# Performance work log

Hardware: AMD Instinct MI355X
Metric: run time of the kernel (lower is better)

## Reference

```python
import jax, jax.numpy as jnp
import numpy as np

H = 8  # pinyin_feature_size = embedding_dim = GRU hidden size
VOCAB = 27


def setup_inputs() -> dict:
    key = jax.random.key(0)
    ks = jax.random.split(key, 10)
    B, T = 131072, 24
    inputs = jax.random.randint(ks[0], (B, T), 0, VOCAB, dtype=jnp.int32)
    emb = jax.random.normal(ks[1], (VOCAB, H), dtype=jnp.float32)
    emb = emb.at[0].set(0.0)  # padding_idx=0
    s = 0.25  # ~ 1/sqrt(hidden) init scale like torch GRU
    w_ih1 = jax.random.normal(ks[2], (3 * H, H), dtype=jnp.float32) * s
    w_hh1 = jax.random.normal(ks[3], (3 * H, H), dtype=jnp.float32) * s
    b_ih1 = jax.random.normal(ks[4], (3 * H,), dtype=jnp.float32) * s
    b_hh1 = jax.random.normal(ks[5], (3 * H,), dtype=jnp.float32) * s
    w_ih2 = jax.random.normal(ks[6], (3 * H, H), dtype=jnp.float32) * s
    w_hh2 = jax.random.normal(ks[7], (3 * H, H), dtype=jnp.float32) * s
    b_ih2 = jax.random.normal(ks[8], (3 * H,), dtype=jnp.float32) * s
    b_hh2 = jax.random.normal(ks[9], (3 * H,), dtype=jnp.float32) * s
    return {"inputs": inputs, "emb": emb,
            "w_ih1": w_ih1, "w_hh1": w_hh1, "b_ih1": b_ih1, "b_hh1": b_hh1,
            "w_ih2": w_ih2, "w_hh2": w_hh2, "b_ih2": b_ih2, "b_hh2": b_hh2}


def _gru_layer(x_seq, w_ih, w_hh, b_ih, b_hh):
    # x_seq: [B, T, H_in] -> all hidden states [B, T, H], final h [B, H]
    B = x_seq.shape[0]
    # precompute input-side gates for all timesteps: [T, B, 3H]
    gi_all = jnp.einsum('bti,gi->tbg', x_seq, w_ih) + b_ih
    h0 = jnp.zeros((B, H), dtype=x_seq.dtype)

    def cell(h, gi):
        gh = h @ w_hh.T + b_hh  # [B, 3H]
        i_r, i_z, i_n = jnp.split(gi, 3, axis=-1)
        h_r, h_z, h_n = jnp.split(gh, 3, axis=-1)
        r = jax.nn.sigmoid(i_r + h_r)
        z = jax.nn.sigmoid(i_z + h_z)
        n = jnp.tanh(i_n + r * h_n)
        h_new = (1.0 - z) * n + z * h
        return h_new, h_new

    h_last, hs = jax.lax.scan(cell, h0, gi_all)
    return jnp.swapaxes(hs, 0, 1), h_last  # [B, T, H], [B, H]


def reference(inputs, emb, w_ih1, w_hh1, b_ih1, b_hh1,
              w_ih2, w_hh2, b_ih2, b_hh2):
    # padding_idx=0 => row 0 of the table is zero
    emb_eff = emb.at[0].set(0.0)
    x = emb_eff[inputs]  # [B, T, H]
    h1_seq, _ = _gru_layer(x, w_ih1, w_hh1, b_ih1, b_hh1)
    # dropout(0.15) between layers is inactive in eval mode
    _, h2_last = _gru_layer(h1_seq, w_ih2, w_hh2, b_ih2, b_hh2)
    return h2_last  # [B, H] == output[1][-1]
```

## Files before the change

### kernel.cpp

```cpp
#include <hip/hip_runtime.h>


typedef __fp16 h2f    __attribute__((ext_vector_type(2)));
typedef __fp16 half8  __attribute__((ext_vector_type(8)));
typedef float  f32x16 __attribute__((ext_vector_type(16)));

#define LOG2E 1.44269504088896f

__device__ __forceinline__ h2f pk2f(float a, float b) {
  return __builtin_amdgcn_cvt_pkrtz(a, b);
}

union H8U { half8 h; unsigned u[4]; h2f p[4]; };

__device__ __forceinline__ unsigned from_upper(unsigned x) {
  auto r = __builtin_amdgcn_permlane32_swap((int)x, (int)x, false, false);
  return (unsigned)r[1];
}

#define MFMA_(A, B, C) __builtin_amdgcn_mfma_f32_32x32x16_f16((A), (B), (C), 0, 0, 0)

__global__ __launch_bounds__(256, 4) void gru2_mfma(
    const int* __restrict__ inputs,
    const float* __restrict__ emb,
    const float* __restrict__ w_ih1, const float* __restrict__ w_hh1,
    const float* __restrict__ b_ih1, const float* __restrict__ b_hh1,
    const float* __restrict__ w_ih2, const float* __restrict__ w_hh2,
    const float* __restrict__ b_ih2, const float* __restrict__ b_hh2,
    float* __restrict__ out)
{
  __shared__ float G1f[27 * 33];
  __shared__ int   TK[128 * 25];

  const int tid   = threadIdx.x;
  const int lane  = tid & 63;
  const int wid   = tid >> 6;
  const int half_ = lane >> 5;
  const int col   = lane & 31;

  for (int idx = tid; idx < 27 * 24; idx += 256) {
    const int tok = idx / 24, g = idx - tok * 24;
    const float s = (g < 16) ? -LOG2E : 2.f * LOG2E;
    float a = b_ih1[g] + ((g < 16) ? b_hh1[g] : 0.f);
    if (tok != 0) {
      #pragma unroll
      for (int j = 0; j < 8; ++j) a = fmaf(w_ih1[g * 8 + j], emb[tok * 8 + j], a);
    }
    G1f[tok * 33 + g] = s * a;
  }

  const long gbase = (long)blockIdx.x * (128 * 24);
  #pragma unroll
  for (int k = 0; k < 12; ++k) {
    const int i = tid + k * 256;
    TK[(i / 24) * 25 + (i % 24)] = inputs[gbase + i];
  }
  __syncthreads();

  const int sl = wid * 32 + col;
  unsigned pkw[4] = {0u, 0u, 0u, 0u};
  #pragma unroll
  for (int t = 0; t < 24; ++t)
    pkw[t / 6] |= ((unsigned)TK[sl * 25 + t]) << (5 * (t % 6));
  const unsigned pk0 = pkw[0], pk1 = pkw[1], pk2_ = pkw[2], pk3 = pkw[3];

  auto loadW = [&](const float* w) -> half8 {
    H8U u;
    u.u[0] = u.u[1] = u.u[2] = u.u[3] = 0u;
    if (half_ == 0 && col < 24) {
      const float s = (col < 16) ? -LOG2E : 2.f * LOG2E;
      const float4* p = (const float4*)(w + col * 8);
      const float4 x = p[0], y = p[1];
      u.p[0] = pk2f(x.x * s, x.y * s);
      u.p[1] = pk2f(x.z * s, x.w * s);
      u.p[2] = pk2f(y.x * s, y.y * s);
      u.p[3] = pk2f(y.z * s, y.w * s);
    }
    return u.h;
  };
  const half8 wa1  = loadW(w_hh1);
  const half8 wa2i = loadW(w_ih2);
  const half8 wa2h = loadW(w_hh2);

  f32x16 c2;
  #pragma unroll
  for (int r = 0; r < 16; ++r) {
    const int m = (r & 3) + 8 * (r >> 2) + 4 * half_;
    float v;
    if (m < 16)      v = -LOG2E * (b_ih2[m] + b_hh2[m]);
    else if (m < 24) v = 2.f * LOG2E * b_hh2[m];
    else             v = 0.f;
    c2[r] = v;
  }
  float bn1[4], bi2n[4];
  #pragma unroll
  for (int i = 0; i < 4; ++i) {
    bn1[i]  = 2.f * LOG2E * b_hh1[16 + 4 * half_ + i];
    bi2n[i] = 2.f * LOG2E * b_ih2[16 + 4 * half_ + i];
  }

  float h1v[4] = {0.f, 0.f, 0.f, 0.f}, h2v[4] = {0.f, 0.f, 0.f, 0.f};
  H8U f1, f2;
  f1.u[0] = f1.u[1] = f1.u[2] = f1.u[3] = 0u;
  f2 = f1;

  const float* g1base = G1f + half_ * 4;

  for (int t6 = 0; t6 < 4; ++t6) {
    const unsigned pw = (t6 == 0) ? pk0 : (t6 == 1) ? pk1 : (t6 == 2) ? pk2_ : pk3;

    #pragma unroll
    for (int j = 0; j < 6; ++j) {
      const unsigned tok = (pw >> (5 * j)) & 31u;
      const float* gp = g1base + tok * 33;

      f32x16 c1;
      c1[0] = gp[0];  c1[1] = gp[1];  c1[2] = gp[2];  c1[3] = gp[3];
      c1[4] = gp[8];  c1[5] = gp[9];  c1[6] = gp[10]; c1[7] = gp[11];
      c1[8] = bn1[0]; c1[9] = bn1[1]; c1[10] = bn1[2]; c1[11] = bn1[3];
      c1[12] = 0.f; c1[13] = 0.f; c1[14] = 0.f; c1[15] = 0.f;

      const f32x16 dh = MFMA_(wa2h, f2.h, c2);
      const f32x16 d1 = MFMA_(wa1, f1.h, c1);

      #pragma unroll
      for (int i = 0; i < 4; ++i) {
        const float r = __builtin_amdgcn_rcpf(1.f + __builtin_amdgcn_exp2f(d1[i]));
        const float z = __builtin_amdgcn_rcpf(1.f + __builtin_amdgcn_exp2f(d1[4 + i]));
        const float na = fmaf(r, d1[8 + i], gp[16 + i]);
        const float n = fmaf(-2.f, __builtin_amdgcn_rcpf(1.f + __builtin_amdgcn_exp2f(na)), 1.f);
        h1v[i] = n + z * (h1v[i] - n);
      }
      {
        const unsigned a = __builtin_bit_cast(unsigned, pk2f(h1v[0], h1v[1]));
        const unsigned b = __builtin_bit_cast(unsigned, pk2f(h1v[2], h1v[3]));
        f1.u[0] = a; f1.u[1] = b;
        f1.u[2] = from_upper(a); f1.u[3] = from_upper(b);
      }

      const f32x16 dg = MFMA_(wa2i, f1.h, dh);

      #pragma unroll
      for (int i = 0; i < 4; ++i) {
        const float r = __builtin_amdgcn_rcpf(1.f + __builtin_amdgcn_exp2f(dg[i]));
        const float z = __builtin_amdgcn_rcpf(1.f + __builtin_amdgcn_exp2f(dg[4 + i]));
        const float gin = dg[8 + i] - dh[8 + i] + bi2n[i];
        const float na = fmaf(r, dh[8 + i], gin);
        const float n = fmaf(-2.f, __builtin_amdgcn_rcpf(1.f + __builtin_amdgcn_exp2f(na)), 1.f);
        h2v[i] = n + z * (h2v[i] - n);
      }
      {
        const unsigned a = __builtin_bit_cast(unsigned, pk2f(h2v[0], h2v[1]));
        const unsigned b = __builtin_bit_cast(unsigned, pk2f(h2v[2], h2v[3]));
        f2.u[0] = a; f2.u[1] = b;
        f2.u[2] = from_upper(a); f2.u[3] = from_upper(b);
      }
    }
  }

  const long seq = (long)blockIdx.x * 128 + sl;
  *(float4*)(out + seq * 8 + 4 * half_) =
      make_float4(h2v[0], h2v[1], h2v[2], h2v[3]);
}

extern "C" void kernel_launch(void* const* d_in, const int* in_sizes, int n_in,
                              void* d_out, int out_size, void* d_ws, size_t ws_size,
                              hipStream_t stream) {
  const int*   inputs = (const int*)d_in[0];
  const float* emb    = (const float*)d_in[1];
  const float* w_ih1  = (const float*)d_in[2];
  const float* w_hh1  = (const float*)d_in[3];
  const float* b_ih1  = (const float*)d_in[4];
  const float* b_hh1  = (const float*)d_in[5];
  const float* w_ih2  = (const float*)d_in[6];
  const float* w_hh2  = (const float*)d_in[7];
  const float* b_ih2  = (const float*)d_in[8];
  const float* b_hh2  = (const float*)d_in[9];
  float* out = (float*)d_out;

  const int B = in_sizes[0] / 24;
  const int grid = B / 128;

  hipLaunchKernelGGL(gru2_mfma, dim3(grid), dim3(256), 0, stream,
                     inputs, emb, w_ih1, w_hh1, b_ih1, b_hh1,
                     w_ih2, w_hh2, b_ih2, b_hh2, out);
}
```

Measured before the change: 114.5 us.

## Prefetch next-step gate table rows and stagger block start with sleeps

Software-pipelines the per-timestep LDS lookups of the precomputed layer-1 input gates: the next token's twelve values are loaded one step ahead into registers while the current step's MFMAs and activations run. It also adds a blockIdx-derived s_sleep stagger at loop start so co-resident waves start out of phase and contend less for the MFMA and transcendental units. The cost is extra registers for the prefetch buffer, which could pressure the 4-block occupancy target, plus a small fixed sleep delay. On the last step it reads a harmless out-of-range token slot.

```diff
diff --git a/kernel.cpp b/kernel.cpp
--- a/kernel.cpp
+++ b/kernel.cpp
@@ -106,28 +106,48 @@
 
   const float* g1base = G1f + half_ * 4;
 
+  {
+    const unsigned key =
+        (blockIdx.x ^ (blockIdx.x >> 3) ^ (blockIdx.x >> 6)) & 7u;
+    if (key & 1u) __builtin_amdgcn_s_sleep(2);
+    if (key & 2u) __builtin_amdgcn_s_sleep(4);
+    if (key & 4u) __builtin_amdgcn_s_sleep(8);
+  }
+
+  float cu[12];
+  {
+    const float* gp = g1base + (pk0 & 31u) * 33;
+    cu[0] = gp[0];  cu[1] = gp[1];  cu[2]  = gp[2];  cu[3]  = gp[3];
+    cu[4] = gp[8];  cu[5] = gp[9];  cu[6]  = gp[10]; cu[7]  = gp[11];
+    cu[8] = gp[16]; cu[9] = gp[17]; cu[10] = gp[18]; cu[11] = gp[19];
+  }
+
   for (int t6 = 0; t6 < 4; ++t6) {
-    const unsigned pw = (t6 == 0) ? pk0 : (t6 == 1) ? pk1 : (t6 == 2) ? pk2_ : pk3;
+    const unsigned pw  = (t6 == 0) ? pk0 : (t6 == 1) ? pk1 : (t6 == 2) ? pk2_ : pk3;
+    const unsigned pwn = (t6 == 0) ? pk1 : (t6 == 1) ? pk2_ : pk3;
 
     #pragma unroll
     for (int j = 0; j < 6; ++j) {
-      const unsigned tok = (pw >> (5 * j)) & 31u;
-      const float* gp = g1base + tok * 33;
-
+      const unsigned tokn = (j < 5) ? ((pw >> (5 * (j + 1))) & 31u) : (pwn & 31u);
+      const float* gq = g1base + tokn * 33;
+      float nx[12];
+      nx[0] = gq[0];  nx[1] = gq[1];  nx[2]  = gq[2];  nx[3]  = gq[3];
+      nx[4] = gq[8];  nx[5] = gq[9];  nx[6]  = gq[10]; nx[7]  = gq[11];
+      nx[8] = gq[16]; nx[9] = gq[17]; nx[10] = gq[18]; nx[11] = gq[19];
+
+      const f32x16 dh = MFMA_(wa2h, f2.h, c2);
       f32x16 c1;
-      c1[0] = gp[0];  c1[1] = gp[1];  c1[2] = gp[2];  c1[3] = gp[3];
-      c1[4] = gp[8];  c1[5] = gp[9];  c1[6] = gp[10]; c1[7] = gp[11];
+      c1[0] = cu[0]; c1[1] = cu[1]; c1[2] = cu[2]; c1[3] = cu[3];
+      c1[4] = cu[4]; c1[5] = cu[5]; c1[6] = cu[6]; c1[7] = cu[7];
       c1[8] = bn1[0]; c1[9] = bn1[1]; c1[10] = bn1[2]; c1[11] = bn1[3];
       c1[12] = 0.f; c1[13] = 0.f; c1[14] = 0.f; c1[15] = 0.f;
-
-      const f32x16 dh = MFMA_(wa2h, f2.h, c2);
       const f32x16 d1 = MFMA_(wa1, f1.h, c1);
 
       #pragma unroll
       for (int i = 0; i < 4; ++i) {
         const float r = __builtin_amdgcn_rcpf(1.f + __builtin_amdgcn_exp2f(d1[i]));
         const float z = __builtin_amdgcn_rcpf(1.f + __builtin_amdgcn_exp2f(d1[4 + i]));
-        const float na = fmaf(r, d1[8 + i], gp[16 + i]);
+        const float na = fmaf(r, d1[8 + i], cu[8 + i]);
         const float n = fmaf(-2.f, __builtin_amdgcn_rcpf(1.f + __builtin_amdgcn_exp2f(na)), 1.f);
         h1v[i] = n + z * (h1v[i] - n);
       }
@@ -155,6 +175,9 @@
         f2.u[0] = a; f2.u[1] = b;
         f2.u[2] = from_upper(a); f2.u[3] = from_upper(b);
       }
+
+      #pragma unroll
+      for (int k = 0; k < 12; ++k) cu[k] = nx[k];
     }
   }
 
```

After: 112.3 us. -2.0%, faster.
